# Performance work log

Hardware: AMD Instinct MI355X
Metric: run time of the kernel (lower is better)

Reference implementation:

```python
import jax, jax.numpy as jnp
import numpy as np

B, D, O, A, H, NL = 1024, 512, 8, 64, 1024, 2

def setup_inputs() -> dict:
    key = jax.random.key(0)
    ks = jax.random.split(key, 8)
    s = 0.02
    return {
        "state": jax.random.normal(ks[0], (B, D), jnp.float32),
        # option network: Linear(D,H) -> ReLU -> Linear(H,O)
        "ow1": jax.random.normal(ks[1], (D, H), jnp.float32) * s, "ob1": jnp.zeros((H,), jnp.float32),
        "ow2": jax.random.normal(ks[2], (H, O), jnp.float32) * s, "ob2": jnp.zeros((O,), jnp.float32),
        # stacked action networks (one per option): Linear(D,H) -> act -> [Linear(H,H) -> act]*(NL-1) -> Linear(H,A)
        "aw1": jax.random.normal(ks[3], (O, D, H), jnp.float32) * s, "ab1": jnp.zeros((O, H), jnp.float32),
        "awh": jax.random.normal(ks[4], (O, NL - 1, H, H), jnp.float32) * s, "abh": jnp.zeros((O, NL - 1, H), jnp.float32),
        "awo": jax.random.normal(ks[5], (O, H, A), jnp.float32) * s, "abo": jnp.zeros((O, A), jnp.float32),
        # termination network: Linear(D,H) -> ReLU -> Linear(H,1) -> Sigmoid
        "tw1": jax.random.normal(ks[6], (D, H), jnp.float32) * s, "tb1": jnp.zeros((H,), jnp.float32),
        "tw2": jax.random.normal(ks[7], (H, 1), jnp.float32) * s, "tb2": jnp.zeros((1,), jnp.float32),
    }

def reference(state, ow1, ob1, ow2, ob2, aw1, ab1, awh, abh, awo, abo, tw1, tb1, tw2, tb2):
    # option routing: softmax over option logits, then per-sample multinomial draw
    opt_logits = jax.nn.relu(state @ ow1 + ob1) @ ow2 + ob2            # [B, O]
    option_probs = jax.nn.softmax(opt_logits, axis=-1)
    # categorical(logits) == multinomial(softmax(logits), 1); fixed key = deterministic reference
    sel = jax.random.categorical(jax.random.key(42), opt_logits, axis=-1)  # [B] int
    # run all experts batched (grouped GEMM), then gather the selected expert's q-values
    h = jax.nn.relu(jnp.einsum('bd,odh->boh', state, aw1) + ab1)       # [B, O, H]
    for i in range(awh.shape[1]):  # fixed small layer count
        h = jax.nn.relu(jnp.einsum('boh,ohg->bog', h, awh[:, i]) + abh[:, i])
    q = jnp.einsum('boh,oha->boa', h, awo) + abo                       # [B, O, A]
    q_sel = jnp.take_along_axis(q, sel[:, None, None], axis=1)[:, 0]   # [B, A]
    action_probs = jax.nn.softmax(q_sel, axis=-1)
    selected_actions = jnp.argmax(action_probs, axis=-1)               # [B]
    termination_prob = jax.nn.sigmoid(jax.nn.relu(state @ tw1 + tb1) @ tw2 + tb2)  # [B, 1]
    return option_probs, action_probs, termination_prob, jnp.argmax(option_probs, axis=-1), selected_actions
```

## Files before the change

kernel.cpp:

```cpp
#include <hip/hip_runtime.h>
#include <math.h>

#define Bsz 1024
#define Din 512
#define Hdim 1024
#define Aact 64
#define MAXT 23
#define NXCD 8

#define OFF_ACT   8192
#define OFF_TERM  73728
#define OFF_OARG  74752
#define OFF_SACT  75776

typedef __attribute__((ext_vector_type(8))) short bf16x8;
typedef __attribute__((ext_vector_type(4))) float f32x4;

__device__ __forceinline__ unsigned rotl32(unsigned x, int d){ return (x << d) | (x >> (32 - d)); }

__device__ __forceinline__ void threefry_042(unsigned& x0, unsigned& x1){
  const unsigned ks0 = 0u, ks1 = 42u, ks2 = 0x1BD11BDAu ^ 0u ^ 42u;
  x0 += ks0; x1 += ks1;
#define TFR(r) { x0 += x1; x1 = rotl32(x1, r); x1 ^= x0; }
  TFR(13) TFR(15) TFR(26) TFR(6)  x0 += ks1; x1 += ks2 + 1u;
  TFR(17) TFR(29) TFR(16) TFR(24) x0 += ks2; x1 += ks0 + 2u;
  TFR(13) TFR(15) TFR(26) TFR(6)  x0 += ks0; x1 += ks1 + 3u;
  TFR(17) TFR(29) TFR(16) TFR(24) x0 += ks1; x1 += ks2 + 4u;
  TFR(13) TFR(15) TFR(26) TFR(6)  x0 += ks2; x1 += ks0 + 5u;
#undef TFR
}

__device__ __forceinline__ float gumbel_at(int idx){
  unsigned x0 = 0u, x1 = (unsigned)idx;
  threefry_042(x0, x1);
  unsigned bits = x0 ^ x1;
  float f = __uint_as_float((bits >> 9) | 0x3F800000u) - 1.0f;
  float u = fmaxf(f, 1.1754944e-38f);
  return -logf(-logf(u));
}

__device__ __forceinline__ unsigned short bf16_rne(float x){
  unsigned u = __float_as_uint(x);
  return (unsigned short)((u + 0x7FFFu + ((u >> 16) & 1u)) >> 16);
}
__device__ __forceinline__ float bf16_tof(unsigned short h){
  return __uint_as_float(((unsigned)h) << 16);
}

__global__ __launch_bounds__(256)
void convert_state(const float* __restrict__ st, unsigned short* __restrict__ hi,
                   unsigned short* __restrict__ lo)
{
  const int i = (blockIdx.x * 256 + threadIdx.x) * 4;
  float4 v = *(const float4*)(st + i);
  ushort4 h, l;
  h.x = bf16_rne(v.x); l.x = bf16_rne(v.x - bf16_tof(h.x));
  h.y = bf16_rne(v.y); l.y = bf16_rne(v.y - bf16_tof(h.y));
  h.z = bf16_rne(v.z); l.z = bf16_rne(v.z - bf16_tof(h.z));
  h.w = bf16_rne(v.w); l.w = bf16_rne(v.w - bf16_tof(h.w));
  *(ushort4*)(hi + i) = h;
  *(ushort4*)(lo + i) = l;
}

template<bool DENSE, bool GATHER, bool HILOOUT>
__global__ __launch_bounds__(256)
void mfma_gemm(const unsigned short* __restrict__ Ahi, const unsigned short* __restrict__ Alo,
               int lda,
               const float* __restrict__ W0, const float* __restrict__ W1, long long wstride,
               const float* __restrict__ b0, const float* __restrict__ b1, int bstride,
               float* __restrict__ C0, float* __restrict__ C1,
               unsigned short* __restrict__ Chi, unsigned short* __restrict__ Clo,
               int N, int K,
               const int* __restrict__ order, const int* __restrict__ offsets,
               const int* __restrict__ tlist)
{
  const float* W; const float* bias; float* C;
  int mbase, r1, n0;
  if (DENSE){
    const int bid = (int)(blockIdx.x + 16u*blockIdx.y + 256u*blockIdx.z);
    const int wf = (bid & 7) * 64 + (bid >> 3);
    const int ny = wf & 15, mx = (wf >> 4) & 15, z = wf >> 8;
    mbase = mx * 64; r1 = Bsz; n0 = ny * 64;
    W = z ? W1 : W0; bias = z ? b1 : b0; C = z ? C1 : C0;
  } else {
    const int bid = (int)(blockIdx.x + gridDim.x * blockIdx.y);
    const int wf = (bid % NXCD) * ((MAXT * 16) / NXCD) + bid / NXCD;
    const int i = wf >> 4;
    if (i >= tlist[0]) return;
    const int o = tlist[1 + 2*i];
    mbase = tlist[2 + 2*i];
    r1 = offsets[o + 1];
    n0 = (wf & 15) * 64;
    W = W0 + (long long)o * wstride; bias = b0 + o * bstride; C = C0;
  }

  __shared__ unsigned short sAh[4096], sAl[4096], sBh[4096], sBl[4096];

  const int tid = threadIdx.x;
  const int wv = tid >> 6, lane = tid & 63;

  const int ar = tid & 63, akb = tid >> 6;
  int grow = mbase + ar;
  int arow = grow < r1 ? grow : mbase;
  if (GATHER) arow = order[arow];
  const unsigned short* pAh = Ahi + (long long)arow * lda;
  const unsigned short* pAl = Alo + (long long)arow * lda;

  const int qr = (wv >> 1) * 32, qc = (wv & 1) * 32;

  f32x4 acc[2][2];
#pragma unroll
  for (int a = 0; a < 2; a++)
#pragma unroll
    for (int b = 0; b < 2; b++) acc[a][b] = (f32x4){0.f, 0.f, 0.f, 0.f};

  for (int kt = 0; kt < K; kt += 64){
#pragma unroll
    for (int h = 0; h < 2; h++){
      const int kb = akb + h*4;
      *(float4*)(sAh + kb*512 + ar*8) = *(const float4*)(pAh + kt + kb*8);
      *(float4*)(sAl + kb*512 + ar*8) = *(const float4*)(pAl + kt + kb*8);
    }
#pragma unroll
    for (int rr = 0; rr < 16; rr++){
      const int kl = wv * 16 + rr;
      const int kb = kl >> 3, e = kl & 7;
      const float v = W[(long long)(kt + kl) * N + n0 + lane];
      const unsigned short h = bf16_rne(v);
      sBh[kb*512 + lane*8 + e] = h;
      sBl[kb*512 + lane*8 + e] = bf16_rne(v - bf16_tof(h));
    }
    __syncthreads();
#pragma unroll
    for (int kg = 0; kg < 2; kg++){
      const int g = (kg*4 + (lane >> 4)) * 512, li = lane & 15;
      bf16x8 a0h = *(const bf16x8*)(sAh + g + (qr + li) * 8);
      bf16x8 a1h = *(const bf16x8*)(sAh + g + (qr + 16 + li) * 8);
      bf16x8 a0l = *(const bf16x8*)(sAl + g + (qr + li) * 8);
      bf16x8 a1l = *(const bf16x8*)(sAl + g + (qr + 16 + li) * 8);
      bf16x8 b0h = *(const bf16x8*)(sBh + g + (qc + li) * 8);
      bf16x8 b1h = *(const bf16x8*)(sBh + g + (qc + 16 + li) * 8);
      bf16x8 b0l = *(const bf16x8*)(sBl + g + (qc + li) * 8);
      bf16x8 b1l = *(const bf16x8*)(sBl + g + (qc + 16 + li) * 8);
      acc[0][0] = __builtin_amdgcn_mfma_f32_16x16x32_bf16(a0h, b0h, acc[0][0], 0, 0, 0);
      acc[0][1] = __builtin_amdgcn_mfma_f32_16x16x32_bf16(a0h, b1h, acc[0][1], 0, 0, 0);
      acc[1][0] = __builtin_amdgcn_mfma_f32_16x16x32_bf16(a1h, b0h, acc[1][0], 0, 0, 0);
      acc[1][1] = __builtin_amdgcn_mfma_f32_16x16x32_bf16(a1h, b1h, acc[1][1], 0, 0, 0);
      acc[0][0] = __builtin_amdgcn_mfma_f32_16x16x32_bf16(a0h, b0l, acc[0][0], 0, 0, 0);
      acc[0][1] = __builtin_amdgcn_mfma_f32_16x16x32_bf16(a0h, b1l, acc[0][1], 0, 0, 0);
      acc[1][0] = __builtin_amdgcn_mfma_f32_16x16x32_bf16(a1h, b0l, acc[1][0], 0, 0, 0);
      acc[1][1] = __builtin_amdgcn_mfma_f32_16x16x32_bf16(a1h, b1l, acc[1][1], 0, 0, 0);
      acc[0][0] = __builtin_amdgcn_mfma_f32_16x16x32_bf16(a0l, b0h, acc[0][0], 0, 0, 0);
      acc[0][1] = __builtin_amdgcn_mfma_f32_16x16x32_bf16(a0l, b1h, acc[0][1], 0, 0, 0);
      acc[1][0] = __builtin_amdgcn_mfma_f32_16x16x32_bf16(a1l, b0h, acc[1][0], 0, 0, 0);
      acc[1][1] = __builtin_amdgcn_mfma_f32_16x16x32_bf16(a1l, b1h, acc[1][1], 0, 0, 0);
    }
    __syncthreads();
  }

#pragma unroll
  for (int rb = 0; rb < 2; rb++)
#pragma unroll
    for (int cb = 0; cb < 2; cb++){
      const int col = n0 + qc + cb*16 + (lane & 15);
      const float bv = bias[col];
#pragma unroll
      for (int r = 0; r < 4; r++){
        const int row = mbase + qr + rb*16 + (lane >> 4)*4 + r;
        if (row < r1){
          const float v = fmaxf(acc[rb][cb][r] + bv, 0.f);
          if (HILOOUT){
            const unsigned short h = bf16_rne(v);
            Chi[(long long)row * N + col] = h;
            Clo[(long long)row * N + col] = bf16_rne(v - bf16_tof(h));
          } else {
            C[(long long)row * N + col] = v;
          }
        }
      }
    }
}

__global__ __launch_bounds__(256)
void head_kernel(const float* __restrict__ h1, const float* __restrict__ th,
                 const float* __restrict__ ow2, const float* __restrict__ ob2,
                 const float* __restrict__ tw2, const float* __restrict__ tb2,
                 float* __restrict__ out, int* __restrict__ sel)
{
  const int b = blockIdx.x;
  const int t = threadIdx.x;
  const float* hrow = h1 + b * Hdim;
  const float* trow = th + b * Hdim;

  float acc[8] = {}; float accT = 0.f;
  for (int k = t; k < Hdim; k += 256){
    float hv = hrow[k];
    const float* w = ow2 + k * 8;
#pragma unroll
    for (int o2 = 0; o2 < 8; ++o2) acc[o2] += hv * w[o2];
    accT += trow[k] * tw2[k];
  }
#pragma unroll
  for (int o2 = 0; o2 < 8; ++o2)
    for (int off = 32; off; off >>= 1) acc[o2] += __shfl_down(acc[o2], off);
  for (int off = 32; off; off >>= 1) accT += __shfl_down(accT, off);

  __shared__ float wred[4][9];
  __shared__ float logits[8];
  __shared__ float gum[8];
  const int wave = t >> 6, lane = t & 63;
  if (lane == 0){
#pragma unroll
    for (int o2 = 0; o2 < 8; ++o2) wred[wave][o2] = acc[o2];
    wred[wave][8] = accT;
  }
  __syncthreads();
  if (t < 9){
    float s = wred[0][t] + wred[1][t] + wred[2][t] + wred[3][t];
    if (t < 8) logits[t] = s + ob2[t];
    else       out[OFF_TERM + b] = 1.f / (1.f + expf(-(s + tb2[0])));
  }
  __syncthreads();
  if (t < 8) gum[t] = logits[t] + gumbel_at(b * 8 + t);
  __syncthreads();
  if (t == 0){
    float m = logits[0]; int am = 0;
#pragma unroll
    for (int o2 = 1; o2 < 8; ++o2) if (logits[o2] > m){ m = logits[o2]; am = o2; }
    float p[8]; float s = 0.f;
#pragma unroll
    for (int o2 = 0; o2 < 8; ++o2){ p[o2] = expf(logits[o2] - m); s += p[o2]; }
    float inv = 1.f / s;
#pragma unroll
    for (int o2 = 0; o2 < 8; ++o2) out[b * 8 + o2] = p[o2] * inv;
    out[OFF_OARG + b] = (float)am;
    float gm = gum[0]; int gs = 0;
#pragma unroll
    for (int o2 = 1; o2 < 8; ++o2) if (gum[o2] > gm){ gm = gum[o2]; gs = o2; }
    sel[b] = gs;
  }
}

__global__ void route_kernel(const int* __restrict__ sel, int* __restrict__ order,
                             int* __restrict__ offsets, int* __restrict__ tlist)
{
  __shared__ int cnt[8];
  __shared__ int base[8];
  const int t = threadIdx.x;
  if (t < 8) cnt[t] = 0;
  __syncthreads();
  const int s = sel[t];
  atomicAdd(&cnt[s], 1);
  __syncthreads();
  if (t == 0){
    int a = 0;
    for (int o = 0; o < 8; ++o){ offsets[o] = a; base[o] = a; a += cnt[o]; }
    offsets[8] = a;
    int nt = 0;
    for (int o = 0; o < 8; ++o)
      for (int mb = offsets[o]; mb < offsets[o] + cnt[o]; mb += 64){
        tlist[1 + 2*nt] = o; tlist[2 + 2*nt] = mb; ++nt;
      }
    tlist[0] = nt;
  }
  __syncthreads();
  const int pos = atomicAdd(&base[s], 1);
  order[pos] = t;
}

__global__ __launch_bounds__(256)
void expert_out_kernel(const float* __restrict__ he2, const float* __restrict__ awo,
                       const float* __restrict__ abo,
                       const int* __restrict__ order, const int* __restrict__ offsets,
                       float* __restrict__ out)
{
  const int r = blockIdx.x;
  int o = 0;
#pragma unroll
  for (int i = 1; i < 8; ++i) if (offsets[i] <= r) o = i;
  const int t = threadIdx.x;
  const int a = t & 63, kg = t >> 6;
  const float* hrow = he2 + r * Hdim;
  const float* W = awo + o * Hdim * Aact;
  float acc = 0.f;
  const int k0 = kg * 256;
  for (int k = k0; k < k0 + 256; ++k) acc += hrow[k] * W[k * Aact + a];
  __shared__ float redm[4][64];
  redm[kg][a] = acc;
  __syncthreads();
  if (t < 64){
    float q = redm[0][a] + redm[1][a] + redm[2][a] + redm[3][a] + abo[o * Aact + a];
    float m = q;
#pragma unroll
    for (int off = 32; off; off >>= 1) m = fmaxf(m, __shfl_xor(m, off));
    float e = expf(q - m);
    float s = e;
#pragma unroll
    for (int off = 32; off; off >>= 1) s += __shfl_xor(s, off);
    const int b = order[r];
    out[OFF_ACT + b * Aact + a] = e / s;
    unsigned long long msk = __ballot(q == m);
    if (a == 0) out[OFF_SACT + b] = (float)__builtin_ctzll(msk);
  }
}

extern "C" void kernel_launch(void* const* d_in, const int* in_sizes, int n_in,
                              void* d_out, int out_size, void* d_ws, size_t ws_size,
                              hipStream_t stream)
{
  (void)in_sizes; (void)n_in; (void)out_size; (void)ws_size;
  const float* state = (const float*)d_in[0];
  const float* ow1   = (const float*)d_in[1];
  const float* ob1   = (const float*)d_in[2];
  const float* ow2   = (const float*)d_in[3];
  const float* ob2   = (const float*)d_in[4];
  const float* aw1   = (const float*)d_in[5];
  const float* ab1   = (const float*)d_in[6];
  const float* awh   = (const float*)d_in[7];
  const float* abh   = (const float*)d_in[8];
  const float* awo   = (const float*)d_in[9];
  const float* abo   = (const float*)d_in[10];
  const float* tw1   = (const float*)d_in[11];
  const float* tb1   = (const float*)d_in[12];
  const float* tw2   = (const float*)d_in[13];
  const float* tb2   = (const float*)d_in[14];
  float* out = (float*)d_out;

  float* h1 = (float*)d_ws;
  float* h2 = h1 + (long long)Bsz * Hdim;
  unsigned short* sthi = (unsigned short*)(h2 + (long long)Bsz * Hdim);
  unsigned short* stlo = sthi + (long long)Bsz * Din;
  unsigned short* h1hi = stlo + (long long)Bsz * Din;
  unsigned short* h1lo = h1hi + (long long)Bsz * Hdim;
  int* sel     = (int*)(h1lo + (long long)Bsz * Hdim);
  int* order   = sel + Bsz;
  int* offsets = order + Bsz;
  int* tlist   = offsets + 9;

  convert_state<<<dim3(512), 256, 0, stream>>>(state, sthi, stlo);
  mfma_gemm<true, false, false><<<dim3(16, 16, 2), 256, 0, stream>>>(
      sthi, stlo, Din, ow1, tw1, 0, ob1, tb1, 0, h1, h2, nullptr, nullptr,
      Hdim, Din, nullptr, nullptr, nullptr);
  head_kernel<<<dim3(Bsz), 256, 0, stream>>>(h1, h2, ow2, ob2, tw2, tb2, out, sel);
  route_kernel<<<dim3(1), 1024, 0, stream>>>(sel, order, offsets, tlist);
  mfma_gemm<false, true, true><<<dim3(MAXT, 16), 256, 0, stream>>>(
      sthi, stlo, Din, aw1, nullptr, (long long)Din*Hdim, ab1, nullptr, Hdim,
      nullptr, nullptr, h1hi, h1lo, Hdim, Din, order, offsets, tlist);
  mfma_gemm<false, false, false><<<dim3(MAXT, 16), 256, 0, stream>>>(
      h1hi, h1lo, Hdim, awh, nullptr, (long long)Hdim*Hdim, abh, nullptr, Hdim,
      h2, nullptr, nullptr, nullptr, Hdim, Hdim, nullptr, offsets, tlist);
  expert_out_kernel<<<dim3(Bsz), 256, 0, stream>>>(h2, awo, abo, order, offsets, out);
}
```

Before: 110.4 us.

## Split-K the expert hidden-layer GEMM and fuse bias-ReLU into output head

The second expert GEMM (K=1024) is split into two K halves launched as a 3D grid, doubling the block count. Each half writes raw partial sums to separate buffers, reusing the h1/h2 scratch. The expert output kernel now sums the two partials, adds the hidden bias and applies ReLU before the final projection. The weight staging loop also packs two bf16 values per 32-bit LDS store. In exchange the partials cost extra global writes and reads, and each block does half the K work, so per-block overhead is amortised over less compute.

```diff
diff --git a/kernel.cpp b/kernel.cpp
--- a/kernel.cpp
+++ b/kernel.cpp
@@ -62,27 +62,28 @@
   *(ushort4*)(lo + i) = l;
 }
 
-template<bool DENSE, bool GATHER, bool HILOOUT>
+template<bool DENSE, bool GATHER, bool HILOOUT, bool RAWPAIR>
 __global__ __launch_bounds__(256)
 void mfma_gemm(const unsigned short* __restrict__ Ahi, const unsigned short* __restrict__ Alo,
                int lda,
                const float* __restrict__ W0, const float* __restrict__ W1, long long wstride,
                const float* __restrict__ b0, const float* __restrict__ b1, int bstride,
                float* __restrict__ C0, float* __restrict__ C1,
+               float* __restrict__ P0,
                unsigned short* __restrict__ Chi, unsigned short* __restrict__ Clo,
                int N, int K,
                const int* __restrict__ order, const int* __restrict__ offsets,
                const int* __restrict__ tlist)
 {
-  const float* W; const float* bias; float* C;
-  int mbase, r1, n0;
+  const float* W; const float* bias = nullptr; float* C;
+  int mbase, r1, n0, kb = 0;
   if (DENSE){
     const int bid = (int)(blockIdx.x + 16u*blockIdx.y + 256u*blockIdx.z);
     const int wf = (bid & 7) * 64 + (bid >> 3);
     const int ny = wf & 15, mx = (wf >> 4) & 15, z = wf >> 8;
     mbase = mx * 64; r1 = Bsz; n0 = ny * 64;
     W = z ? W1 : W0; bias = z ? b1 : b0; C = z ? C1 : C0;
-  } else {
+  } else if (!RAWPAIR){
     const int bid = (int)(blockIdx.x + gridDim.x * blockIdx.y);
     const int wf = (bid % NXCD) * ((MAXT * 16) / NXCD) + bid / NXCD;
     const int i = wf >> 4;
@@ -92,6 +93,18 @@
     r1 = offsets[o + 1];
     n0 = (wf & 15) * 64;
     W = W0 + (long long)o * wstride; bias = b0 + o * bstride; C = C0;
+  } else {
+    const int bid = (int)(blockIdx.x + 23u*blockIdx.y + 368u*blockIdx.z);
+    const int wf = (bid & 7) * 92 + (bid >> 3);
+    kb = wf / 368; const int rem = wf - kb * 368;
+    const int i = rem >> 4;
+    if (i >= tlist[0]) return;
+    const int o = tlist[1 + 2*i];
+    mbase = tlist[2 + 2*i];
+    r1 = offsets[o + 1];
+    n0 = (rem & 15) * 64;
+    W = W0 + (long long)o * wstride;
+    C = kb ? P0 : C0;
   }
 
   __shared__ unsigned short sAh[4096], sAl[4096], sBh[4096], sBl[4096];
@@ -114,21 +127,26 @@
 #pragma unroll
     for (int b = 0; b < 2; b++) acc[a][b] = (f32x4){0.f, 0.f, 0.f, 0.f};
 
-  for (int kt = 0; kt < K; kt += 64){
+  const int kbeg = RAWPAIR ? kb * (K >> 1) : 0;
+  const int kend = RAWPAIR ? kbeg + (K >> 1) : K;
+
+  for (int kt = kbeg; kt < kend; kt += 64){
 #pragma unroll
     for (int h = 0; h < 2; h++){
-      const int kb = akb + h*4;
-      *(float4*)(sAh + kb*512 + ar*8) = *(const float4*)(pAh + kt + kb*8);
-      *(float4*)(sAl + kb*512 + ar*8) = *(const float4*)(pAl + kt + kb*8);
+      const int kbl = akb + h*4;
+      *(float4*)(sAh + kbl*512 + ar*8) = *(const float4*)(pAh + kt + kbl*8);
+      *(float4*)(sAl + kbl*512 + ar*8) = *(const float4*)(pAl + kt + kbl*8);
     }
 #pragma unroll
-    for (int rr = 0; rr < 16; rr++){
-      const int kl = wv * 16 + rr;
-      const int kb = kl >> 3, e = kl & 7;
-      const float v = W[(long long)(kt + kl) * N + n0 + lane];
-      const unsigned short h = bf16_rne(v);
-      sBh[kb*512 + lane*8 + e] = h;
-      sBl[kb*512 + lane*8 + e] = bf16_rne(v - bf16_tof(h));
+    for (int rp = 0; rp < 8; rp++){
+      const int kl = wv * 16 + rp * 2;
+      const int kbl = kl >> 3, e = kl & 7;
+      const float v0 = W[(long long)(kt + kl) * N + n0 + lane];
+      const float v1 = W[(long long)(kt + kl + 1) * N + n0 + lane];
+      const unsigned short h0 = bf16_rne(v0), h1 = bf16_rne(v1);
+      const unsigned short l0 = bf16_rne(v0 - bf16_tof(h0)), l1 = bf16_rne(v1 - bf16_tof(h1));
+      *(unsigned*)(sBh + kbl*512 + lane*8 + e) = ((unsigned)h1 << 16) | h0;
+      *(unsigned*)(sBl + kbl*512 + lane*8 + e) = ((unsigned)l1 << 16) | l0;
     }
     __syncthreads();
 #pragma unroll
@@ -163,18 +181,22 @@
 #pragma unroll
     for (int cb = 0; cb < 2; cb++){
       const int col = n0 + qc + cb*16 + (lane & 15);
-      const float bv = bias[col];
+      const float bv = RAWPAIR ? 0.f : bias[col];
 #pragma unroll
       for (int r = 0; r < 4; r++){
         const int row = mbase + qr + rb*16 + (lane >> 4)*4 + r;
         if (row < r1){
-          const float v = fmaxf(acc[rb][cb][r] + bv, 0.f);
-          if (HILOOUT){
-            const unsigned short h = bf16_rne(v);
-            Chi[(long long)row * N + col] = h;
-            Clo[(long long)row * N + col] = bf16_rne(v - bf16_tof(h));
+          if (RAWPAIR){
+            C[(long long)row * N + col] = acc[rb][cb][r];
           } else {
-            C[(long long)row * N + col] = v;
+            const float v = fmaxf(acc[rb][cb][r] + bv, 0.f);
+            if (HILOOUT){
+              const unsigned short h = bf16_rne(v);
+              Chi[(long long)row * N + col] = h;
+              Clo[(long long)row * N + col] = bf16_rne(v - bf16_tof(h));
+            } else {
+              C[(long long)row * N + col] = v;
+            }
           }
         }
       }
@@ -269,8 +291,9 @@
 }
 
 __global__ __launch_bounds__(256)
-void expert_out_kernel(const float* __restrict__ he2, const float* __restrict__ awo,
-                       const float* __restrict__ abo,
+void expert_out_kernel(const float* __restrict__ ba, const float* __restrict__ bb,
+                       const float* __restrict__ abh,
+                       const float* __restrict__ awo, const float* __restrict__ abo,
                        const int* __restrict__ order, const int* __restrict__ offsets,
                        float* __restrict__ out)
 {
@@ -280,11 +303,15 @@
   for (int i = 1; i < 8; ++i) if (offsets[i] <= r) o = i;
   const int t = threadIdx.x;
   const int a = t & 63, kg = t >> 6;
-  const float* hrow = he2 + r * Hdim;
-  const float* W = awo + o * Hdim * Aact;
+  const long long rb = (long long)r * Hdim;
+  const float* ab = abh + (long long)o * Hdim;
+  const float* W = awo + (long long)o * Hdim * Aact;
   float acc = 0.f;
   const int k0 = kg * 256;
-  for (int k = k0; k < k0 + 256; ++k) acc += hrow[k] * W[k * Aact + a];
+  for (int k = k0; k < k0 + 256; ++k){
+    float hv = fmaxf(ba[rb + k] + bb[rb + k] + ab[k], 0.f);
+    acc += hv * W[k * Aact + a];
+  }
   __shared__ float redm[4][64];
   redm[kg][a] = acc;
   __syncthreads();
@@ -338,16 +365,17 @@
   int* tlist   = offsets + 9;
 
   convert_state<<<dim3(512), 256, 0, stream>>>(state, sthi, stlo);
-  mfma_gemm<true, false, false><<<dim3(16, 16, 2), 256, 0, stream>>>(
-      sthi, stlo, Din, ow1, tw1, 0, ob1, tb1, 0, h1, h2, nullptr, nullptr,
+  mfma_gemm<true, false, false, false><<<dim3(16, 16, 2), 256, 0, stream>>>(
+      sthi, stlo, Din, ow1, tw1, 0, ob1, tb1, 0, h1, h2, nullptr, nullptr, nullptr,
       Hdim, Din, nullptr, nullptr, nullptr);
   head_kernel<<<dim3(Bsz), 256, 0, stream>>>(h1, h2, ow2, ob2, tw2, tb2, out, sel);
   route_kernel<<<dim3(1), 1024, 0, stream>>>(sel, order, offsets, tlist);
-  mfma_gemm<false, true, true><<<dim3(MAXT, 16), 256, 0, stream>>>(
+  mfma_gemm<false, true, true, false><<<dim3(MAXT, 16), 256, 0, stream>>>(
       sthi, stlo, Din, aw1, nullptr, (long long)Din*Hdim, ab1, nullptr, Hdim,
-      nullptr, nullptr, h1hi, h1lo, Hdim, Din, order, offsets, tlist);
-  mfma_gemm<false, false, false><<<dim3(MAXT, 16), 256, 0, stream>>>(
-      h1hi, h1lo, Hdim, awh, nullptr, (long long)Hdim*Hdim, abh, nullptr, Hdim,
-      h2, nullptr, nullptr, nullptr, Hdim, Hdim, nullptr, offsets, tlist);
-  expert_out_kernel<<<dim3(Bsz), 256, 0, stream>>>(h2, awo, abo, order, offsets, out);
-}
+      nullptr, nullptr, nullptr, h1hi, h1lo, Hdim, Din, order, offsets, tlist);
+  mfma_gemm<false, false, false, true><<<dim3(MAXT, 16, 2), 256, 0, stream>>>(
+      h1hi, h1lo, Hdim, awh, nullptr, (long long)Hdim*Hdim, nullptr, nullptr, 0,
+      h1, nullptr, h2, nullptr, nullptr, Hdim, Hdim, nullptr, offsets, tlist);
+  expert_out_kernel<<<dim3(Bsz), 256, 0, stream>>>(
+      h1, h2, abh, awo, abo, order, offsets, out);
+}
```

After: 111.0 us. No clear change (+0.6%).

## Move expert output layer to split-K MFMA and pack B-tile LDS stores

Applied to the files above, without the earlier changes.

Replaces the scalar FP32 per-row expert output kernel with a grouped MFMA GEMM using hi/lo bf16 splitting and split-K over four partitions. A small kernel then sums the partials and computes softmax and argmax. The second hidden layer now writes hi/lo bf16 outputs instead of fp32, and the weight-tile conversion writes two bf16 values per 32-bit LDS store. This adds a kernel launch and a partial-sum buffer in exchange for removing the slow scalar FMA loop.

```diff
diff --git a/kernel.cpp b/kernel.cpp
--- a/kernel.cpp
+++ b/kernel.cpp
@@ -117,18 +117,20 @@
   for (int kt = 0; kt < K; kt += 64){
 #pragma unroll
     for (int h = 0; h < 2; h++){
-      const int kb = akb + h*4;
-      *(float4*)(sAh + kb*512 + ar*8) = *(const float4*)(pAh + kt + kb*8);
-      *(float4*)(sAl + kb*512 + ar*8) = *(const float4*)(pAl + kt + kb*8);
-    }
-#pragma unroll
-    for (int rr = 0; rr < 16; rr++){
-      const int kl = wv * 16 + rr;
-      const int kb = kl >> 3, e = kl & 7;
-      const float v = W[(long long)(kt + kl) * N + n0 + lane];
-      const unsigned short h = bf16_rne(v);
-      sBh[kb*512 + lane*8 + e] = h;
-      sBl[kb*512 + lane*8 + e] = bf16_rne(v - bf16_tof(h));
+      const int kbl = akb + h*4;
+      *(float4*)(sAh + kbl*512 + ar*8) = *(const float4*)(pAh + kt + kbl*8);
+      *(float4*)(sAl + kbl*512 + ar*8) = *(const float4*)(pAl + kt + kbl*8);
+    }
+#pragma unroll
+    for (int rp = 0; rp < 8; rp++){
+      const int kl = wv * 16 + rp * 2;
+      const int kbl = kl >> 3, e = kl & 7;
+      const float v0 = W[(long long)(kt + kl) * N + n0 + lane];
+      const float v1 = W[(long long)(kt + kl + 1) * N + n0 + lane];
+      const unsigned short h0 = bf16_rne(v0), h1 = bf16_rne(v1);
+      const unsigned short l0 = bf16_rne(v0 - bf16_tof(h0)), l1 = bf16_rne(v1 - bf16_tof(h1));
+      *(unsigned*)(sBh + kbl*512 + lane*8 + e) = ((unsigned)h1 << 16) | h0;
+      *(unsigned*)(sBl + kbl*512 + lane*8 + e) = ((unsigned)l1 << 16) | l0;
     }
     __syncthreads();
 #pragma unroll
@@ -182,6 +184,125 @@
 }
 
 __global__ __launch_bounds__(256)
+void q_mfma(const unsigned short* __restrict__ Ahi, const unsigned short* __restrict__ Alo,
+            const float* __restrict__ awo,
+            float* __restrict__ qp,
+            const int* __restrict__ offsets, const int* __restrict__ tlist)
+{
+  const int i = blockIdx.x;
+  if (i >= tlist[0]) return;
+  const int o = tlist[1 + 2*i];
+  const int mbase = tlist[2 + 2*i];
+  const int r1 = offsets[o + 1];
+  const int kb = blockIdx.y;
+  const float* W = awo + (long long)o * Hdim * Aact;
+
+  __shared__ unsigned short sAh[4096], sAl[4096], sBh[4096], sBl[4096];
+
+  const int tid = threadIdx.x;
+  const int wv = tid >> 6, lane = tid & 63;
+  const int ar = tid & 63, akb = tid >> 6;
+  int grow = mbase + ar;
+  int arow = grow < r1 ? grow : mbase;
+  const unsigned short* pAh = Ahi + (long long)arow * Hdim;
+  const unsigned short* pAl = Alo + (long long)arow * Hdim;
+
+  const int qr = (wv >> 1) * 32, qc = (wv & 1) * 32;
+
+  f32x4 acc[2][2];
+#pragma unroll
+  for (int a = 0; a < 2; a++)
+#pragma unroll
+    for (int b = 0; b < 2; b++) acc[a][b] = (f32x4){0.f, 0.f, 0.f, 0.f};
+
+  const int kbeg = kb * 256, kend = kbeg + 256;
+  for (int kt = kbeg; kt < kend; kt += 64){
+#pragma unroll
+    for (int h = 0; h < 2; h++){
+      const int kbl = akb + h*4;
+      *(float4*)(sAh + kbl*512 + ar*8) = *(const float4*)(pAh + kt + kbl*8);
+      *(float4*)(sAl + kbl*512 + ar*8) = *(const float4*)(pAl + kt + kbl*8);
+    }
+#pragma unroll
+    for (int rp = 0; rp < 8; rp++){
+      const int kl = wv * 16 + rp * 2;
+      const int kbl = kl >> 3, e = kl & 7;
+      const float v0 = W[(kt + kl) * Aact + lane];
+      const float v1 = W[(kt + kl + 1) * Aact + lane];
+      const unsigned short h0 = bf16_rne(v0), h1 = bf16_rne(v1);
+      const unsigned short l0 = bf16_rne(v0 - bf16_tof(h0)), l1 = bf16_rne(v1 - bf16_tof(h1));
+      *(unsigned*)(sBh + kbl*512 + lane*8 + e) = ((unsigned)h1 << 16) | h0;
+      *(unsigned*)(sBl + kbl*512 + lane*8 + e) = ((unsigned)l1 << 16) | l0;
+    }
+    __syncthreads();
+#pragma unroll
+    for (int kg = 0; kg < 2; kg++){
+      const int g = (kg*4 + (lane >> 4)) * 512, li = lane & 15;
+      bf16x8 a0h = *(const bf16x8*)(sAh + g + (qr + li) * 8);
+      bf16x8 a1h = *(const bf16x8*)(sAh + g + (qr + 16 + li) * 8);
+      bf16x8 a0l = *(const bf16x8*)(sAl + g + (qr + li) * 8);
+      bf16x8 a1l = *(const bf16x8*)(sAl + g + (qr + 16 + li) * 8);
+      bf16x8 b0h = *(const bf16x8*)(sBh + g + (qc + li) * 8);
+      bf16x8 b1h = *(const bf16x8*)(sBh + g + (qc + 16 + li) * 8);
+      bf16x8 b0l = *(const bf16x8*)(sBl + g + (qc + li) * 8);
+      bf16x8 b1l = *(const bf16x8*)(sBl + g + (qc + 16 + li) * 8);
+      acc[0][0] = __builtin_amdgcn_mfma_f32_16x16x32_bf16(a0h, b0h, acc[0][0], 0, 0, 0);
+      acc[0][1] = __builtin_amdgcn_mfma_f32_16x16x32_bf16(a0h, b1h, acc[0][1], 0, 0, 0);
+      acc[1][0] = __builtin_amdgcn_mfma_f32_16x16x32_bf16(a1h, b0h, acc[1][0], 0, 0, 0);
+      acc[1][1] = __builtin_amdgcn_mfma_f32_16x16x32_bf16(a1h, b1h, acc[1][1], 0, 0, 0);
+      acc[0][0] = __builtin_amdgcn_mfma_f32_16x16x32_bf16(a0h, b0l, acc[0][0], 0, 0, 0);
+      acc[0][1] = __builtin_amdgcn_mfma_f32_16x16x32_bf16(a0h, b1l, acc[0][1], 0, 0, 0);
+      acc[1][0] = __builtin_amdgcn_mfma_f32_16x16x32_bf16(a1h, b0l, acc[1][0], 0, 0, 0);
+      acc[1][1] = __builtin_amdgcn_mfma_f32_16x16x32_bf16(a1h, b1l, acc[1][1], 0, 0, 0);
+      acc[0][0] = __builtin_amdgcn_mfma_f32_16x16x32_bf16(a0l, b0h, acc[0][0], 0, 0, 0);
+      acc[0][1] = __builtin_amdgcn_mfma_f32_16x16x32_bf16(a0l, b1h, acc[0][1], 0, 0, 0);
+      acc[1][0] = __builtin_amdgcn_mfma_f32_16x16x32_bf16(a1l, b0h, acc[1][0], 0, 0, 0);
+      acc[1][1] = __builtin_amdgcn_mfma_f32_16x16x32_bf16(a1l, b1h, acc[1][1], 0, 0, 0);
+    }
+    __syncthreads();
+  }
+
+#pragma unroll
+  for (int rb = 0; rb < 2; rb++)
+#pragma unroll
+    for (int cb = 0; cb < 2; cb++){
+      const int col = qc + cb*16 + (lane & 15);
+#pragma unroll
+      for (int r = 0; r < 4; r++){
+        const int row = mbase + qr + rb*16 + (lane >> 4)*4 + r;
+        if (row < r1)
+          qp[((long long)kb * Bsz + row) * Aact + col] = acc[rb][cb][r];
+      }
+    }
+}
+
+__global__ __launch_bounds__(64)
+void act_kernel(const float* __restrict__ qp, const float* __restrict__ abo,
+                const int* __restrict__ order, const int* __restrict__ offsets,
+                float* __restrict__ out)
+{
+  const int r = blockIdx.x;
+  int o = 0;
+#pragma unroll
+  for (int i = 1; i < 8; ++i) if (offsets[i] <= r) o = i;
+  const int a = threadIdx.x;
+  const long long idx = (long long)r * Aact + a;
+  float q = qp[idx] + qp[(long long)Bsz*Aact + idx] + qp[2ll*Bsz*Aact + idx]
+          + qp[3ll*Bsz*Aact + idx] + abo[o * Aact + a];
+  float m = q;
+#pragma unroll
+  for (int off = 32; off; off >>= 1) m = fmaxf(m, __shfl_xor(m, off));
+  float e = expf(q - m);
+  float s = e;
+#pragma unroll
+  for (int off = 32; off; off >>= 1) s += __shfl_xor(s, off);
+  const int b = order[r];
+  out[OFF_ACT + b * Aact + a] = e / s;
+  unsigned long long msk = __ballot(q == m);
+  if (a == 0) out[OFF_SACT + b] = (float)__builtin_ctzll(msk);
+}
+
+__global__ __launch_bounds__(256)
 void head_kernel(const float* __restrict__ h1, const float* __restrict__ th,
                  const float* __restrict__ ow2, const float* __restrict__ ob2,
                  const float* __restrict__ tw2, const float* __restrict__ tb2,
@@ -266,42 +387,6 @@
   __syncthreads();
   const int pos = atomicAdd(&base[s], 1);
   order[pos] = t;
-}
-
-__global__ __launch_bounds__(256)
-void expert_out_kernel(const float* __restrict__ he2, const float* __restrict__ awo,
-                       const float* __restrict__ abo,
-                       const int* __restrict__ order, const int* __restrict__ offsets,
-                       float* __restrict__ out)
-{
-  const int r = blockIdx.x;
-  int o = 0;
-#pragma unroll
-  for (int i = 1; i < 8; ++i) if (offsets[i] <= r) o = i;
-  const int t = threadIdx.x;
-  const int a = t & 63, kg = t >> 6;
-  const float* hrow = he2 + r * Hdim;
-  const float* W = awo + o * Hdim * Aact;
-  float acc = 0.f;
-  const int k0 = kg * 256;
-  for (int k = k0; k < k0 + 256; ++k) acc += hrow[k] * W[k * Aact + a];
-  __shared__ float redm[4][64];
-  redm[kg][a] = acc;
-  __syncthreads();
-  if (t < 64){
-    float q = redm[0][a] + redm[1][a] + redm[2][a] + redm[3][a] + abo[o * Aact + a];
-    float m = q;
-#pragma unroll
-    for (int off = 32; off; off >>= 1) m = fmaxf(m, __shfl_xor(m, off));
-    float e = expf(q - m);
-    float s = e;
-#pragma unroll
-    for (int off = 32; off; off >>= 1) s += __shfl_xor(s, off);
-    const int b = order[r];
-    out[OFF_ACT + b * Aact + a] = e / s;
-    unsigned long long msk = __ballot(q == m);
-    if (a == 0) out[OFF_SACT + b] = (float)__builtin_ctzll(msk);
-  }
 }
 
 extern "C" void kernel_launch(void* const* d_in, const int* in_sizes, int n_in,
@@ -328,11 +413,14 @@
 
   float* h1 = (float*)d_ws;
   float* h2 = h1 + (long long)Bsz * Hdim;
-  unsigned short* sthi = (unsigned short*)(h2 + (long long)Bsz * Hdim);
+  float* qp = h2 + (long long)Bsz * Hdim;
+  unsigned short* sthi = (unsigned short*)(qp + 4ll * Bsz * Aact);
   unsigned short* stlo = sthi + (long long)Bsz * Din;
   unsigned short* h1hi = stlo + (long long)Bsz * Din;
   unsigned short* h1lo = h1hi + (long long)Bsz * Hdim;
-  int* sel     = (int*)(h1lo + (long long)Bsz * Hdim);
+  unsigned short* h2hi = h1lo + (long long)Bsz * Hdim;
+  unsigned short* h2lo = h2hi + (long long)Bsz * Hdim;
+  int* sel     = (int*)(h2lo + (long long)Bsz * Hdim);
   int* order   = sel + Bsz;
   int* offsets = order + Bsz;
   int* tlist   = offsets + 9;
@@ -346,8 +434,9 @@
   mfma_gemm<false, true, true><<<dim3(MAXT, 16), 256, 0, stream>>>(
       sthi, stlo, Din, aw1, nullptr, (long long)Din*Hdim, ab1, nullptr, Hdim,
       nullptr, nullptr, h1hi, h1lo, Hdim, Din, order, offsets, tlist);
-  mfma_gemm<false, false, false><<<dim3(MAXT, 16), 256, 0, stream>>>(
+  mfma_gemm<false, false, true><<<dim3(MAXT, 16), 256, 0, stream>>>(
       h1hi, h1lo, Hdim, awh, nullptr, (long long)Hdim*Hdim, abh, nullptr, Hdim,
-      h2, nullptr, nullptr, nullptr, Hdim, Hdim, nullptr, offsets, tlist);
-  expert_out_kernel<<<dim3(Bsz), 256, 0, stream>>>(h2, awo, abo, order, offsets, out);
-}
+      nullptr, nullptr, h2hi, h2lo, Hdim, Hdim, nullptr, offsets, tlist);
+  q_mfma<<<dim3(MAXT, 4), 256, 0, stream>>>(h2hi, h2lo, awo, qp, offsets, tlist);
+  act_kernel<<<dim3(Bsz), 64, 0, stream>>>(qp, abo, order, offsets, out);
+}
```

After: 101.7 us (median of 2 runs). 1.09x faster.
